# Kernel optimization log

Measured on AMD Instinct MI355X. Metric: run time of the kernel, lower is better.

## Reference

```python
import jax, jax.numpy as jnp
import numpy as np
from functools import partial

H = 2048   # image height
W = 2048   # image width
FC_IN = 1024
FC_OUT = 10


def setup_inputs() -> dict:
    key = jax.random.key(0)
    ks = jax.random.split(key, 7)
    x = jax.random.normal(ks[0], (1, H, W), dtype=jnp.float32)
    # Conv2d(1,1,1): scalar weight + bias
    w_in = jax.random.normal(ks[1], (1, 1, 1, 1), dtype=jnp.float32)
    b_in = jax.random.normal(ks[2], (1,), dtype=jnp.float32) * 0.1
    # Conv1d(1,1,2,padding=1): 2-tap kernel + bias
    w_state = jax.random.normal(ks[3], (1, 1, 2), dtype=jnp.float32) * 0.5
    b_state = jax.random.normal(ks[4], (1,), dtype=jnp.float32) * 0.1
    # Linear(1024, 10)
    fc_w = jax.random.normal(ks[5], (FC_OUT, FC_IN), dtype=jnp.float32) * (1.0 / np.sqrt(FC_IN))
    fc_b = jax.random.normal(ks[6], (FC_OUT,), dtype=jnp.float32) * 0.1
    return {"x": x, "w_in": w_in, "b_in": b_in, "w_state": w_state,
            "b_state": b_state, "fc_w": fc_w, "fc_b": fc_b}


def reference(x, w_in, b_in, w_state, b_state, fc_w, fc_b):
    img = x[0]                      # [H, W]
    h_dim, w_dim = img.shape
    w_skew = w_dim + h_dim - 1      # skewed image width

    # --- skew: row r shifted right by r, zero-filled elsewhere ---
    rows = jnp.arange(h_dim)[:, None]          # [H,1]
    cols = jnp.arange(w_dim)[None, :] + rows   # [H,W] destination columns
    skewed = jnp.zeros((h_dim, w_skew), dtype=img.dtype).at[rows, cols].set(img)

    # --- 1x1 input convolution: scalar affine ---
    input_matrix = skewed * w_in[0, 0, 0, 0] + b_in[0]   # [H, Wskew]

    k0 = w_state[0, 0, 0]
    k1 = w_state[0, 0, 1]
    bs = b_state[0]

    # --- sequential column scan: h_c = tanh(k0*shift(h) + k1*h + bs + inp_c) ---
    def step(h, inp_col):
        shifted = jnp.concatenate([jnp.zeros((1,), h.dtype), h[:-1]])
        a = jnp.tanh(k0 * shifted + k1 * h + bs + inp_col)
        return a, a

    h0 = jnp.zeros((h_dim,), dtype=img.dtype)
    _, acts = jax.lax.scan(step, h0, input_matrix.T)     # acts: [Wskew, H]

    # --- unskew: unskewed[r, c] = acts[r + c, r] ---
    c_idx = jnp.arange(w_dim)[None, :]                   # [1, W]
    unskewed = acts[rows + c_idx, rows]                  # [H, W]

    flat = unskewed.reshape(-1, FC_IN)                   # [H*W/1024, 1024]
    return flat @ fc_w.T + fc_b                          # [H*W/1024, 10]
```

## Files before the change

### kernel.cpp

```cpp
#include <hip/hip_runtime.h>

#define HH 2048
#define WW 2048
#define WSK 4095
#define WSKP 4096
#define BLKS 8
#define NW  4
#define NT  (NW * 64)
#define KCH 32
#define NCH (WSKP / KCH)
#define FC_IN 1024
#define FC_OUT 10
#define NFLAT ((HH * WW) / FC_IN)

__device__ __forceinline__ float tanh_pre(float xs) {
  float e = __builtin_amdgcn_exp2f(xs);
  float r = __builtin_amdgcn_rcpf(e + 1.0f);
  return __builtin_fmaf(-2.0f, r, 1.0f);
}

__device__ __forceinline__ float wave_shr1(float src, float old) {
  int r = __builtin_amdgcn_update_dpp(
      __builtin_bit_cast(int, old), __builtin_bit_cast(int, src),
      0x138 , 0xF, 0xF, false);
  return __builtin_bit_cast(float, r);
}

__global__ __launch_bounds__(256) void skew_kernel(
    const float* __restrict__ img, const float* __restrict__ w_in,
    const float* __restrict__ b_in, const float* __restrict__ b_state,
    float* __restrict__ inp) {
  const float S = 2.88539008177792681472f;
  const float ws = w_in[0] * S;
  const float Cs = (b_in[0] + b_state[0]) * S;
  int gid = blockIdx.x * 256 + threadIdx.x;
  int r = gid & (HH - 1);
  int c = gid >> 11;
  int idx = c - r;
  float v = Cs;
  if ((unsigned)idx < (unsigned)WW) v = fmaf(ws, img[(size_t)r * WW + idx], Cs);
  inp[gid] = v;
}

__global__ __launch_bounds__(NT) void scan_kernel(
    const float* __restrict__ w_state, const float* __restrict__ inp,
    float* __restrict__ acts, unsigned* __restrict__ flags) {
  const int t = threadIdx.x;
  const int wv = t >> 6;
  const int lane = t & 63;
  const int blk = blockIdx.x;
  const int r = blk * NT + t;

  const float S = 2.88539008177792681472f;
  const float k0s = w_state[0] * S;
  const float k1s = w_state[1] * S;

  __shared__ float ring[2][NW][KCH];

  float h = 0.0f;
  const float* colp_in = inp + r;
  float* colp_out = acts + r;

  float pf[KCH];
  #pragma unroll
  for (int d = 0; d < KCH; ++d) pf[d] = colp_in[(size_t)d * HH];

  const unsigned* upflag = flags + (blk - 1) * NCH;
  unsigned* myflag = flags + blk * NCH;
  const float* uprow = acts + (blk * NT - 1);

  for (int e = 0; e < NCH + NW - 1; ++e) {
    const int ch = e - wv;
    if (0 <= ch && ch < NCH) {
      const int c0 = ch * KCH;

      float bvec;
      if (wv == 0) {
        bvec = 0.0f;
        if (blk > 0) {
          const unsigned want = (unsigned)(ch + 1);
          while (__hip_atomic_load(upflag + ch, __ATOMIC_ACQUIRE,
                                   __HIP_MEMORY_SCOPE_AGENT) != want)
            __builtin_amdgcn_s_sleep(1);
          int cl = c0 + lane - 1;
          if (lane < KCH && cl >= 0) bvec = uprow[(size_t)cl * HH];
        }
      } else {
        bvec = ring[(e & 1) ^ 1][wv - 1][lane & (KCH - 1)];
      }
      if (lane == 63) ring[e & 1][wv][0] = h;

      const int cb = (ch + 1 < NCH ? ch + 1 : ch) * KCH;

      #pragma unroll
      for (int cc = 0; cc < KCH; ++cc) {
        float cur = pf[cc];
        pf[cc] = colp_in[(size_t)(cb + cc) * HH];

        float pv = __builtin_bit_cast(float,
            __builtin_amdgcn_readlane(__builtin_bit_cast(int, bvec), cc));
        float prev = wave_shr1(h, pv);

        h = tanh_pre(fmaf(k0s, prev, fmaf(k1s, h, cur)));

        if (lane == 63 && cc + 1 < KCH) ring[e & 1][wv][cc + 1] = h;
        colp_out[(size_t)(c0 + cc) * HH] = h;
      }

      if (wv == NW - 1 && lane == 63)
        __hip_atomic_store(myflag + ch, (unsigned)(ch + 1), __ATOMIC_RELEASE,
                           __HIP_MEMORY_SCOPE_AGENT);
    }
    asm volatile("s_waitcnt lgkmcnt(0)\n\ts_barrier" ::: "memory");
  }
}

__global__ __launch_bounds__(64) void fc_kernel(
    const float* __restrict__ acts, const float* __restrict__ fc_w,
    const float* __restrict__ fc_b, float* __restrict__ out) {
  const int i = blockIdx.x;
  const int lane = threadIdx.x;
  const int r = i >> 1;
  const int base = (i & 1) << 10;

  float acc[FC_OUT];
  #pragma unroll
  for (int j = 0; j < FC_OUT; ++j) acc[j] = 0.0f;

  for (int k = lane; k < FC_IN; k += 64) {
    float v = acts[(size_t)(r + base + k) * HH + r];
    #pragma unroll
    for (int j = 0; j < FC_OUT; ++j)
      acc[j] = fmaf(v, fc_w[j * FC_IN + k], acc[j]);
  }

  #pragma unroll
  for (int j = 0; j < FC_OUT; ++j) {
    #pragma unroll
    for (int off = 32; off > 0; off >>= 1)
      acc[j] += __shfl_down(acc[j], off);
  }

  if (lane == 0) {
    #pragma unroll
    for (int j = 0; j < FC_OUT; ++j)
      out[i * FC_OUT + j] = acc[j] + fc_b[j];
  }
}

extern "C" void kernel_launch(void* const* d_in, const int* in_sizes, int n_in,
                              void* d_out, int out_size, void* d_ws, size_t ws_size,
                              hipStream_t stream) {
  const float* x       = (const float*)d_in[0];
  const float* w_in    = (const float*)d_in[1];
  const float* b_in    = (const float*)d_in[2];
  const float* w_state = (const float*)d_in[3];
  const float* b_state = (const float*)d_in[4];
  const float* fc_w    = (const float*)d_in[5];
  const float* fc_b    = (const float*)d_in[6];
  float* out = (float*)d_out;
  float* buf = (float*)d_ws;

  unsigned* flags = (unsigned*)d_out;

  skew_kernel<<<(WSKP * HH) / 256, 256, 0, stream>>>(x, w_in, b_in, b_state, buf);
  scan_kernel<<<BLKS, NT, 0, stream>>>(w_state, buf, buf, flags);
  fc_kernel<<<NFLAT, 64, 0, stream>>>(buf, fc_w, fc_b, out);
}
```

Measured before the change: 556.4 us.

## Replace per-chunk flag handoff with tagged mailbox ring and tile FC reads

Cross-block handoff in the scan changes. Instead of a per-chunk acquire/release flag followed by a global read of the upstream row, the last wave now publishes each boundary value packed with its column tag into a 64-bit mailbox ring. The consumer polls those tagged slots with relaxed atomics and prefetches the next chunk's slots. A backpressure wait stops the ring from overwriting slots that have not been consumed. The FC kernel is also restructured: each block handles 16 rows, keeps the FC weights in LDS and stages coalesced column tiles of the activations, replacing strided gathers. The risks are that tags sitting in the reused output buffer could alias by chance, and that the FC kernel now does more redundant predicated iterations.

```diff
diff --git a/kernel.cpp b/kernel.cpp
--- a/kernel.cpp
+++ b/kernel.cpp
@@ -12,6 +12,8 @@
 #define FC_IN 1024
 #define FC_OUT 10
 #define NFLAT ((HH * WW) / FC_IN)
+
+#define MRING 2048
 
 __device__ __forceinline__ float tanh_pre(float xs) {
   float e = __builtin_amdgcn_exp2f(xs);
@@ -44,7 +46,7 @@
 
 __global__ __launch_bounds__(NT) void scan_kernel(
     const float* __restrict__ w_state, const float* __restrict__ inp,
-    float* __restrict__ acts, unsigned* __restrict__ flags) {
+    float* __restrict__ acts, unsigned long long* __restrict__ mbox) {
   const int t = threadIdx.x;
   const int wv = t >> 6;
   const int lane = t & 63;
@@ -65,9 +67,13 @@
   #pragma unroll
   for (int d = 0; d < KCH; ++d) pf[d] = colp_in[(size_t)d * HH];
 
-  const unsigned* upflag = flags + (blk - 1) * NCH;
-  unsigned* myflag = flags + blk * NCH;
-  const float* uprow = acts + (blk * NT - 1);
+  unsigned long long praw = 0;
+  if (wv == 0 && blk > 0 && lane < KCH) {
+    unsigned long long* mb_up = mbox + (size_t)(blk - 1) * MRING;
+    int cl = lane - 1;
+    praw = __hip_atomic_load(&mb_up[cl & (MRING - 1)], __ATOMIC_RELAXED,
+                             __HIP_MEMORY_SCOPE_AGENT);
+  }
 
   for (int e = 0; e < NCH + NW - 1; ++e) {
     const int ch = e - wv;
@@ -78,19 +84,46 @@
       if (wv == 0) {
         bvec = 0.0f;
         if (blk > 0) {
-          const unsigned want = (unsigned)(ch + 1);
-          while (__hip_atomic_load(upflag + ch, __ATOMIC_ACQUIRE,
-                                   __HIP_MEMORY_SCOPE_AGENT) != want)
+          unsigned long long* mb_up = mbox + (size_t)(blk - 1) * MRING;
+          const int cl = c0 + lane - 1;
+          const bool need = (lane < KCH) && (cl >= 0);
+          const unsigned want = (unsigned)(cl + 1);
+          unsigned long long raw = praw;
+          while (!__all((!need) || ((unsigned)(raw >> 32) == want))) {
             __builtin_amdgcn_s_sleep(1);
-          int cl = c0 + lane - 1;
-          if (lane < KCH && cl >= 0) bvec = uprow[(size_t)cl * HH];
+            if (need)
+              raw = __hip_atomic_load(&mb_up[cl & (MRING - 1)],
+                                      __ATOMIC_RELAXED,
+                                      __HIP_MEMORY_SCOPE_AGENT);
+          }
+          if (need) bvec = __builtin_bit_cast(float, (unsigned)raw);
+          if (lane < KCH)
+            praw = __hip_atomic_load(&mb_up[(cl + KCH) & (MRING - 1)],
+                                     __ATOMIC_RELAXED,
+                                     __HIP_MEMORY_SCOPE_AGENT);
         }
       } else {
         bvec = ring[(e & 1) ^ 1][wv - 1][lane & (KCH - 1)];
       }
-      if (lane == 63) ring[e & 1][wv][0] = h;
+      if (lane == 63 && wv != NW - 1) ring[e & 1][wv][0] = h;
+
+      if (wv == NW - 1 && blk + 1 < BLKS) {
+        const int cmax = c0 + KCH - 1;
+        if (cmax >= MRING) {
+          unsigned long long* mb_dn = mbox + (size_t)(blk + 1) * MRING;
+          const int cref = cmax - (MRING - 128);
+          const unsigned wantt = (unsigned)(cref + 1);
+          if (lane == 63) {
+            while ((unsigned)(__hip_atomic_load(&mb_dn[cref & (MRING - 1)],
+                       __ATOMIC_RELAXED, __HIP_MEMORY_SCOPE_AGENT) >> 32)
+                   != wantt)
+              __builtin_amdgcn_s_sleep(8);
+          }
+        }
+      }
 
       const int cb = (ch + 1 < NCH ? ch + 1 : ch) * KCH;
+      unsigned long long* mb_my = mbox + (size_t)blk * MRING;
 
       #pragma unroll
       for (int cc = 0; cc < KCH; ++cc) {
@@ -103,48 +136,89 @@
 
         h = tanh_pre(fmaf(k0s, prev, fmaf(k1s, h, cur)));
 
-        if (lane == 63 && cc + 1 < KCH) ring[e & 1][wv][cc + 1] = h;
+        if (lane == 63) {
+          if (wv != NW - 1) {
+            if (cc + 1 < KCH) ring[e & 1][wv][cc + 1] = h;
+          } else {
+            unsigned long long pack =
+                ((unsigned long long)(unsigned)(c0 + cc + 1) << 32) |
+                (unsigned long long)__builtin_bit_cast(unsigned, h);
+            __hip_atomic_store(&mb_my[(c0 + cc) & (MRING - 1)], pack,
+                               __ATOMIC_RELAXED, __HIP_MEMORY_SCOPE_AGENT);
+          }
+        }
         colp_out[(size_t)(c0 + cc) * HH] = h;
       }
-
-      if (wv == NW - 1 && lane == 63)
-        __hip_atomic_store(myflag + ch, (unsigned)(ch + 1), __ATOMIC_RELEASE,
-                           __HIP_MEMORY_SCOPE_AGENT);
     }
     asm volatile("s_waitcnt lgkmcnt(0)\n\ts_barrier" ::: "memory");
   }
 }
 
-__global__ __launch_bounds__(64) void fc_kernel(
+#define FCR 16
+#define FCCH 256
+#define FCT 256
+
+__global__ __launch_bounds__(FCT) void fc_kernel(
     const float* __restrict__ acts, const float* __restrict__ fc_w,
     const float* __restrict__ fc_b, float* __restrict__ out) {
-  const int i = blockIdx.x;
-  const int lane = threadIdx.x;
-  const int r = i >> 1;
-  const int base = (i & 1) << 10;
+  __shared__ float fcw[FC_OUT * FC_IN];
+  __shared__ float tile[FCCH][FCR + 1];
+
+  const int tid = threadIdx.x;
+  const int bb = blockIdx.x;
+  const int r0 = bb * FCR;
+
+  for (int i = tid; i < FC_OUT * FC_IN; i += FCT) fcw[i] = fc_w[i];
+
+  const int il = tid >> 3;
+  const int cs = tid & 7;
+  const int rloc = il >> 1;
+  const int koff = (r0 + rloc) + ((il & 1) << 10);
+
+  const int lrr = tid & 15;
+  const int lco = tid >> 4;
 
   float acc[FC_OUT];
   #pragma unroll
   for (int j = 0; j < FC_OUT; ++j) acc[j] = 0.0f;
 
-  for (int k = lane; k < FC_IN; k += 64) {
-    float v = acts[(size_t)(r + base + k) * HH + r];
+  __syncthreads();
+
+  const int cend = r0 + FCR - 1 + 2047;
+  for (int cb = r0; cb <= cend; cb += FCCH) {
     #pragma unroll
-    for (int j = 0; j < FC_OUT; ++j)
-      acc[j] = fmaf(v, fc_w[j * FC_IN + k], acc[j]);
+    for (int s = 0; s < FCCH / 16; ++s) {
+      int cc = s * 16 + lco;
+      int col = cb + cc;
+      int colc = col < WSK ? col : (WSK - 1);
+      tile[cc][lrr] = acts[(size_t)colc * HH + r0 + lrr];
+    }
+    __syncthreads();
+
+    #pragma unroll 4
+    for (int tt = 0; tt < FCCH / 8; ++tt) {
+      int cc = tt * 8 + cs;
+      int k = cb + cc - koff;
+      if (0 <= k && k < FC_IN) {
+        float v = tile[cc][rloc];
+        #pragma unroll
+        for (int j = 0; j < FC_OUT; ++j)
+          acc[j] = fmaf(v, fcw[j * FC_IN + k], acc[j]);
+      }
+    }
+    __syncthreads();
   }
 
   #pragma unroll
   for (int j = 0; j < FC_OUT; ++j) {
+    acc[j] += __shfl_down(acc[j], 4, 8);
+    acc[j] += __shfl_down(acc[j], 2, 8);
+    acc[j] += __shfl_down(acc[j], 1, 8);
+  }
+  if (cs == 0) {
+    const int i = bb * 32 + il;
     #pragma unroll
-    for (int off = 32; off > 0; off >>= 1)
-      acc[j] += __shfl_down(acc[j], off);
-  }
-
-  if (lane == 0) {
-    #pragma unroll
-    for (int j = 0; j < FC_OUT; ++j)
-      out[i * FC_OUT + j] = acc[j] + fc_b[j];
+    for (int j = 0; j < FC_OUT; ++j) out[i * FC_OUT + j] = acc[j] + fc_b[j];
   }
 }
 
@@ -161,9 +235,9 @@
   float* out = (float*)d_out;
   float* buf = (float*)d_ws;
 
-  unsigned* flags = (unsigned*)d_out;
+  unsigned long long* mbox = (unsigned long long*)d_out;
 
   skew_kernel<<<(WSKP * HH) / 256, 256, 0, stream>>>(x, w_in, b_in, b_state, buf);
-  scan_kernel<<<BLKS, NT, 0, stream>>>(w_state, buf, buf, flags);
-  fc_kernel<<<NFLAT, 64, 0, stream>>>(buf, fc_w, fc_b, out);
-}
+  scan_kernel<<<BLKS, NT, 0, stream>>>(w_state, buf, buf, mbox);
+  fc_kernel<<<HH / FCR, FCT, 0, stream>>>(buf, fc_w, fc_b, out);
+}
```

Measured after the change: 643.4 us. +15.6%, slower.

## Switch scan buffers to row-major with float4 I/O and shared-memory FC weights

Applied to the files above, without the earlier changes.

The skewed input/activation buffer changes from column-major to row-major, so each scan thread reads and writes its own row in float4 chunks. The FC kernel can then read contiguous rows instead of striding by the image height, and it caches fc_w in LDS and handles four outputs per block. The inter-block flag protocol is reordered: the boundary for the next chunk is fetched before the current results are stored, and flags are published one iteration later, after the stores. The trade-off is that per-thread row accesses are no longer coalesced across lanes, which may raise memory traffic on the latency-bound scan.

```diff
diff --git a/kernel.cpp b/kernel.cpp
--- a/kernel.cpp
+++ b/kernel.cpp
@@ -11,7 +11,7 @@
 #define NCH (WSKP / KCH)
 #define FC_IN 1024
 #define FC_OUT 10
-#define NFLAT ((HH * WW) / FC_IN)
+
 
 __device__ __forceinline__ float tanh_pre(float xs) {
   float e = __builtin_amdgcn_exp2f(xs);
@@ -25,6 +25,10 @@
       0x138 , 0xF, 0xF, false);
   return __builtin_bit_cast(float, r);
 }
+
+#define PFE(cc) ((cc & 3) == 0 ? pf[cc >> 2].x : \
+                 (cc & 3) == 1 ? pf[cc >> 2].y : \
+                 (cc & 3) == 2 ? pf[cc >> 2].z : pf[cc >> 2].w)
 
 __global__ __launch_bounds__(256) void skew_kernel(
     const float* __restrict__ img, const float* __restrict__ w_in,
@@ -34,8 +38,8 @@
   const float ws = w_in[0] * S;
   const float Cs = (b_in[0] + b_state[0]) * S;
   int gid = blockIdx.x * 256 + threadIdx.x;
-  int r = gid & (HH - 1);
-  int c = gid >> 11;
+  int c = gid & (WSKP - 1);
+  int r = gid >> 12;
   int idx = c - r;
   float v = Cs;
   if ((unsigned)idx < (unsigned)WW) v = fmaf(ws, img[(size_t)r * WW + idx], Cs);
@@ -58,80 +62,121 @@
   __shared__ float ring[2][NW][KCH];
 
   float h = 0.0f;
-  const float* colp_in = inp + r;
-  float* colp_out = acts + r;
-
-  float pf[KCH];
+  const float* inrow = inp + (size_t)r * WSKP;
+  float* myrow = acts + (size_t)r * WSKP;
+
+  float4 pf[KCH / 4];
   #pragma unroll
-  for (int d = 0; d < KCH; ++d) pf[d] = colp_in[(size_t)d * HH];
+  for (int q = 0; q < KCH / 4; ++q)
+    pf[q] = *(const float4*)(inrow + 4 * q);
 
   const unsigned* upflag = flags + (blk - 1) * NCH;
   unsigned* myflag = flags + blk * NCH;
-  const float* uprow = acts + (blk * NT - 1);
+  const float* uprow = acts + ((size_t)(blk * NT) - 1) * WSKP;
+
+  float bvec = 0.0f;
+  if (wv == 0 && blk > 0) {
+    while (__hip_atomic_load(upflag + 1, __ATOMIC_ACQUIRE,
+                             __HIP_MEMORY_SCOPE_AGENT) != 2u)
+      __builtin_amdgcn_s_sleep(2);
+    int cl = lane - 1;
+    if (lane < KCH && cl >= 0) bvec = uprow[cl];
+  }
 
   for (int e = 0; e < NCH + NW - 1; ++e) {
+    if (wv == NW - 1 && blk + 1 < BLKS && lane == 63) {
+      int chp = e - NW;
+      if (chp >= 0)
+        __hip_atomic_store(myflag + chp, (unsigned)(chp + 1),
+                           __ATOMIC_RELEASE, __HIP_MEMORY_SCOPE_AGENT);
+    }
+
     const int ch = e - wv;
     if (0 <= ch && ch < NCH) {
       const int c0 = ch * KCH;
 
-      float bvec;
+      float bv;
       if (wv == 0) {
-        bvec = 0.0f;
-        if (blk > 0) {
-          const unsigned want = (unsigned)(ch + 1);
-          while (__hip_atomic_load(upflag + ch, __ATOMIC_ACQUIRE,
-                                   __HIP_MEMORY_SCOPE_AGENT) != want)
-            __builtin_amdgcn_s_sleep(1);
-          int cl = c0 + lane - 1;
-          if (lane < KCH && cl >= 0) bvec = uprow[(size_t)cl * HH];
-        }
+        bv = bvec;
       } else {
-        bvec = ring[(e & 1) ^ 1][wv - 1][lane & (KCH - 1)];
-      }
-      if (lane == 63) ring[e & 1][wv][0] = h;
-
-      const int cb = (ch + 1 < NCH ? ch + 1 : ch) * KCH;
+        bv = ring[(e & 1) ^ 1][wv - 1][lane & (KCH - 1)];
+      }
+
+      const float h0 = h;
+      float hbuf[KCH];
+      const float* nx = inrow + (ch + 1 < NCH ? (ch + 1) : ch) * KCH;
 
       #pragma unroll
       for (int cc = 0; cc < KCH; ++cc) {
-        float cur = pf[cc];
-        pf[cc] = colp_in[(size_t)(cb + cc) * HH];
+        float cur = PFE(cc);
+        if ((cc & 3) == 3)
+          pf[cc >> 2] = *(const float4*)(nx + (cc & ~3));
 
         float pv = __builtin_bit_cast(float,
-            __builtin_amdgcn_readlane(__builtin_bit_cast(int, bvec), cc));
+            __builtin_amdgcn_readlane(__builtin_bit_cast(int, bv), cc));
         float prev = wave_shr1(h, pv);
 
         h = tanh_pre(fmaf(k0s, prev, fmaf(k1s, h, cur)));
-
-        if (lane == 63 && cc + 1 < KCH) ring[e & 1][wv][cc + 1] = h;
-        colp_out[(size_t)(c0 + cc) * HH] = h;
-      }
-
-      if (wv == NW - 1 && lane == 63)
-        __hip_atomic_store(myflag + ch, (unsigned)(ch + 1), __ATOMIC_RELEASE,
-                           __HIP_MEMORY_SCOPE_AGENT);
+        hbuf[cc] = h;
+      }
+
+      if (wv == 0 && blk > 0 && ch + 1 < NCH) {
+        const unsigned want = (unsigned)(ch + 2);
+        while (__hip_atomic_load(upflag + ch + 1, __ATOMIC_ACQUIRE,
+                                 __HIP_MEMORY_SCOPE_AGENT) != want)
+          __builtin_amdgcn_s_sleep(1);
+        bvec = 0.0f;
+        if (lane < KCH) bvec = uprow[(ch + 1) * KCH + lane - 1];
+      }
+
+      #pragma unroll
+      for (int q = 0; q < KCH / 4; ++q) {
+        float4 s;
+        s.x = hbuf[4 * q + 0]; s.y = hbuf[4 * q + 1];
+        s.z = hbuf[4 * q + 2]; s.w = hbuf[4 * q + 3];
+        *(float4*)(myrow + c0 + 4 * q) = s;
+      }
+
+      if (lane == 63 && wv != NW - 1) {
+        float* rp = &ring[e & 1][wv][0];
+        rp[0] = h0;
+        #pragma unroll
+        for (int i = 1; i < KCH; ++i) rp[i] = hbuf[i - 1];
+      }
     }
     asm volatile("s_waitcnt lgkmcnt(0)\n\ts_barrier" ::: "memory");
   }
-}
-
-__global__ __launch_bounds__(64) void fc_kernel(
+
+  if (wv == NW - 1 && blk + 1 < BLKS && lane == 63)
+    __hip_atomic_store(myflag + (NCH - 1), (unsigned)NCH,
+                       __ATOMIC_RELEASE, __HIP_MEMORY_SCOPE_AGENT);
+}
+
+#define FCT 256
+__global__ __launch_bounds__(FCT) void fc_kernel(
     const float* __restrict__ acts, const float* __restrict__ fc_w,
     const float* __restrict__ fc_b, float* __restrict__ out) {
-  const int i = blockIdx.x;
-  const int lane = threadIdx.x;
+  __shared__ float fcw[FC_OUT * FC_IN];
+  const int tid = threadIdx.x;
+  for (int i = tid; i < FC_OUT * FC_IN; i += FCT) fcw[i] = fc_w[i];
+  __syncthreads();
+
+  const int wv = tid >> 6;
+  const int lane = tid & 63;
+  const int i = blockIdx.x * 4 + wv;
   const int r = i >> 1;
-  const int base = (i & 1) << 10;
+  const float* arow = acts + (size_t)r * WSKP + r + ((i & 1) << 10);
 
   float acc[FC_OUT];
   #pragma unroll
   for (int j = 0; j < FC_OUT; ++j) acc[j] = 0.0f;
 
+  #pragma unroll 4
   for (int k = lane; k < FC_IN; k += 64) {
-    float v = acts[(size_t)(r + base + k) * HH + r];
+    float v = arow[k];
     #pragma unroll
     for (int j = 0; j < FC_OUT; ++j)
-      acc[j] = fmaf(v, fc_w[j * FC_IN + k], acc[j]);
+      acc[j] = fmaf(v, fcw[j * FC_IN + k], acc[j]);
   }
 
   #pragma unroll
@@ -140,7 +185,6 @@
     for (int off = 32; off > 0; off >>= 1)
       acc[j] += __shfl_down(acc[j], off);
   }
-
   if (lane == 0) {
     #pragma unroll
     for (int j = 0; j < FC_OUT; ++j)
@@ -163,7 +207,7 @@
 
   unsigned* flags = (unsigned*)d_out;
 
-  skew_kernel<<<(WSKP * HH) / 256, 256, 0, stream>>>(x, w_in, b_in, b_state, buf);
+  skew_kernel<<<(HH * WSKP) / 256, 256, 0, stream>>>(x, w_in, b_in, b_state, buf);
   scan_kernel<<<BLKS, NT, 0, stream>>>(w_state, buf, buf, flags);
-  fc_kernel<<<NFLAT, 64, 0, stream>>>(buf, fc_w, fc_b, out);
-}
+  fc_kernel<<<(HH * WW / FC_IN) / 4, FCT, 0, stream>>>(buf, fc_w, fc_b, out);
+}
```

Result: slower. 575.6 us (+3.4%).

## Fuse FC projection into scan kernel and write only boundary activations

Applied to the files above, without the earlier changes.

The FC layer is folded into the scan. Each thread accumulates its unskewed activations against fc_w, which is staged in shared memory, and emits output rows when a 1024-element segment completes, so the separate fc_kernel and its strided reads of the acts buffer go away. The scan now stores only the last row of each block (the boundary needed by the next block), not the full activation matrix. Flags move into the workspace with a memset, and the inter-block wait is prefetched one chunk ahead. The cost is extra FMA work and LDS reads inside the serial scan loop, which lies on the critical path.

```diff
diff --git a/kernel.cpp b/kernel.cpp
--- a/kernel.cpp
+++ b/kernel.cpp
@@ -11,7 +11,9 @@
 #define NCH (WSKP / KCH)
 #define FC_IN 1024
 #define FC_OUT 10
-#define NFLAT ((HH * WW) / FC_IN)
+
+typedef float f32x4 __attribute__((ext_vector_type(4)));
+
 
 __device__ __forceinline__ float tanh_pre(float xs) {
   float e = __builtin_amdgcn_exp2f(xs);
@@ -24,6 +26,11 @@
       __builtin_bit_cast(int, old), __builtin_bit_cast(int, src),
       0x138 , 0xF, 0xF, false);
   return __builtin_bit_cast(float, r);
+}
+
+__device__ __forceinline__ float rlane(float v, int l) {
+  return __builtin_bit_cast(float,
+      __builtin_amdgcn_readlane(__builtin_bit_cast(int, v), l));
 }
 
 __global__ __launch_bounds__(256) void skew_kernel(
@@ -39,23 +46,37 @@
   int idx = c - r;
   float v = Cs;
   if ((unsigned)idx < (unsigned)WW) v = fmaf(ws, img[(size_t)r * WW + idx], Cs);
-  inp[gid] = v;
+  if (c != WSKP - 1) inp[gid] = v;
 }
 
 __global__ __launch_bounds__(NT) void scan_kernel(
     const float* __restrict__ w_state, const float* __restrict__ inp,
-    float* __restrict__ acts, unsigned* __restrict__ flags) {
+    float* __restrict__ acts, const float* __restrict__ fc_w,
+    const float* __restrict__ fc_b, float* __restrict__ out,
+    unsigned* __restrict__ flags) {
   const int t = threadIdx.x;
   const int wv = t >> 6;
   const int lane = t & 63;
   const int blk = blockIdx.x;
   const int r = blk * NT + t;
+  const int w0 = blk * NT + wv * 64;
 
   const float S = 2.88539008177792681472f;
   const float k0s = w_state[0] * S;
   const float k1s = w_state[1] * S;
 
   __shared__ float ring[2][NW][KCH];
+  __shared__ float fcw[FC_OUT * FC_IN];
+
+  for (int i = t; i < (FC_OUT * FC_IN) / 4; i += NT)
+    ((f32x4*)fcw)[i] = ((const f32x4*)fc_w)[i];
+  float fcb[FC_OUT];
+  #pragma unroll
+  for (int j = 0; j < FC_OUT; ++j) fcb[j] = fc_b[j];
+
+  float acc[FC_OUT];
+  #pragma unroll
+  for (int j = 0; j < FC_OUT; ++j) acc[j] = 0.0f;
 
   float h = 0.0f;
   const float* colp_in = inp + r;
@@ -67,85 +88,90 @@
 
   const unsigned* upflag = flags + (blk - 1) * NCH;
   unsigned* myflag = flags + blk * NCH;
-  const float* uprow = acts + (blk * NT - 1);
+  const float* uprow = blk > 0 ? acts + (blk * NT - 1) : acts;
+
+  __syncthreads();
+
+  float bvec = 0.0f;
+  if (wv == 0 && blk > 0) {
+    while (__hip_atomic_load(upflag + 1, __ATOMIC_ACQUIRE,
+                             __HIP_MEMORY_SCOPE_AGENT) != 2u)
+      __builtin_amdgcn_s_sleep(2);
+    if (lane >= 1 && lane < KCH) bvec = uprow[(size_t)(lane - 1) * HH];
+  }
+
+  const bool pub = (wv == NW - 1) && (lane == 63);
+  const bool rw = (lane == 63) && (wv != NW - 1);
 
   for (int e = 0; e < NCH + NW - 1; ++e) {
+    if (wv == NW - 1 && blk + 1 < BLKS && lane == 63) {
+      int chp = e - NW;
+      if (chp >= 0)
+        __hip_atomic_store(myflag + chp, (unsigned)(chp + 1),
+                           __ATOMIC_RELEASE, __HIP_MEMORY_SCOPE_AGENT);
+    }
+
     const int ch = e - wv;
     if (0 <= ch && ch < NCH) {
       const int c0 = ch * KCH;
-
-      float bvec;
-      if (wv == 0) {
-        bvec = 0.0f;
-        if (blk > 0) {
-          const unsigned want = (unsigned)(ch + 1);
-          while (__hip_atomic_load(upflag + ch, __ATOMIC_ACQUIRE,
-                                   __HIP_MEMORY_SCOPE_AGENT) != want)
-            __builtin_amdgcn_s_sleep(1);
-          int cl = c0 + lane - 1;
-          if (lane < KCH && cl >= 0) bvec = uprow[(size_t)cl * HH];
-        }
-      } else {
-        bvec = ring[(e & 1) ^ 1][wv - 1][lane & (KCH - 1)];
-      }
-      if (lane == 63) ring[e & 1][wv][0] = h;
+      float bv = (wv == 0) ? bvec
+                           : ring[(e & 1) ^ 1][wv - 1][lane & (KCH - 1)];
+      if (rw) ring[e & 1][wv][0] = h;
 
       const int cb = (ch + 1 < NCH ? ch + 1 : ch) * KCH;
+
+      const bool rel = (c0 + KCH - 1 >= w0) && (c0 <= w0 + 63 + 2047);
 
       #pragma unroll
       for (int cc = 0; cc < KCH; ++cc) {
         float cur = pf[cc];
         pf[cc] = colp_in[(size_t)(cb + cc) * HH];
 
-        float pv = __builtin_bit_cast(float,
-            __builtin_amdgcn_readlane(__builtin_bit_cast(int, bvec), cc));
+        float pv = rlane(bv, cc);
         float prev = wave_shr1(h, pv);
-
         h = tanh_pre(fmaf(k0s, prev, fmaf(k1s, h, cur)));
 
-        if (lane == 63 && cc + 1 < KCH) ring[e & 1][wv][cc + 1] = h;
-        colp_out[(size_t)(c0 + cc) * HH] = h;
+        if (rw && cc + 1 < KCH) ring[e & 1][wv][cc + 1] = h;
+        if (pub && c0 + cc < WSK) colp_out[(size_t)(c0 + cc) * HH] = h;
+
+        if (rel) {
+          int k01 = (c0 + cc) - r;
+          bool inr = (unsigned)k01 < 2048u;
+          float hv = inr ? h : 0.0f;
+          int kk = k01 & 1023;
+          #pragma unroll
+          for (int j = 0; j < FC_OUT; ++j)
+            acc[j] = fmaf(hv, fcw[j * FC_IN + kk], acc[j]);
+          bool crossed = inr && (kk == 1023);
+          if (__any(crossed ? 1 : 0)) {
+            if (crossed) {
+              int i2 = 2 * r + (k01 >> 10);
+              #pragma unroll
+              for (int j = 0; j < FC_OUT; ++j) {
+                out[i2 * FC_OUT + j] = acc[j] + fcb[j];
+                acc[j] = 0.0f;
+              }
+            }
+          }
+        }
       }
 
-      if (wv == NW - 1 && lane == 63)
-        __hip_atomic_store(myflag + ch, (unsigned)(ch + 1), __ATOMIC_RELEASE,
-                           __HIP_MEMORY_SCOPE_AGENT);
+      if (wv == 0 && blk > 0 && ch + 1 < NCH) {
+        const unsigned want = (unsigned)(ch + 2);
+        while (__hip_atomic_load(upflag + ch + 1, __ATOMIC_ACQUIRE,
+                                 __HIP_MEMORY_SCOPE_AGENT) != want)
+          __builtin_amdgcn_s_sleep(1);
+        bvec = 0.0f;
+        if (lane < KCH)
+          bvec = uprow[(size_t)((ch + 1) * KCH + lane - 1) * HH];
+      }
     }
     asm volatile("s_waitcnt lgkmcnt(0)\n\ts_barrier" ::: "memory");
   }
-}
 
-__global__ __launch_bounds__(64) void fc_kernel(
-    const float* __restrict__ acts, const float* __restrict__ fc_w,
-    const float* __restrict__ fc_b, float* __restrict__ out) {
-  const int i = blockIdx.x;
-  const int lane = threadIdx.x;
-  const int r = i >> 1;
-  const int base = (i & 1) << 10;
-
-  float acc[FC_OUT];
-  #pragma unroll
-  for (int j = 0; j < FC_OUT; ++j) acc[j] = 0.0f;
-
-  for (int k = lane; k < FC_IN; k += 64) {
-    float v = acts[(size_t)(r + base + k) * HH + r];
-    #pragma unroll
-    for (int j = 0; j < FC_OUT; ++j)
-      acc[j] = fmaf(v, fc_w[j * FC_IN + k], acc[j]);
-  }
-
-  #pragma unroll
-  for (int j = 0; j < FC_OUT; ++j) {
-    #pragma unroll
-    for (int off = 32; off > 0; off >>= 1)
-      acc[j] += __shfl_down(acc[j], off);
-  }
-
-  if (lane == 0) {
-    #pragma unroll
-    for (int j = 0; j < FC_OUT; ++j)
-      out[i * FC_OUT + j] = acc[j] + fc_b[j];
-  }
+  if (wv == NW - 1 && blk + 1 < BLKS && lane == 63)
+    __hip_atomic_store(myflag + (NCH - 1), (unsigned)NCH,
+                       __ATOMIC_RELEASE, __HIP_MEMORY_SCOPE_AGENT);
 }
 
 extern "C" void kernel_launch(void* const* d_in, const int* in_sizes, int n_in,
@@ -161,9 +187,9 @@
   float* out = (float*)d_out;
   float* buf = (float*)d_ws;
 
-  unsigned* flags = (unsigned*)d_out;
+  unsigned* flags = (unsigned*)(buf + (size_t)(WSKP - 1) * HH);
+  hipMemsetAsync(flags, 0, BLKS * NCH * sizeof(unsigned), stream);
 
   skew_kernel<<<(WSKP * HH) / 256, 256, 0, stream>>>(x, w_in, b_in, b_state, buf);
-  scan_kernel<<<BLKS, NT, 0, stream>>>(w_state, buf, buf, flags);
-  fc_kernel<<<NFLAT, 64, 0, stream>>>(buf, fc_w, fc_b, out);
+  scan_kernel<<<BLKS, NT, 0, stream>>>(w_state, buf, buf, fc_w, fc_b, out, flags);
 }
```

Measured after the change: 1.123 ms. +101.8%, slower.
